# Kernel tuning notes

Hardware: AMD Instinct MI355X
Metric: run time of the kernel (lower is better)

The kernel has to match this reference:

```python
import jax, jax.numpy as jnp
import numpy as np

N = 10000      # nodes
E = 50000      # edges
NS = 48        # multiplicity of 0e (scalars)
NV = 10        # multiplicity of 1o (vectors)
NEF = 128      # n_edge_features
HID = 128      # hidden_features
W1N = NS * NS  # path 0e x 0e -> 0e
W2N = NS * NV  # path 0e x 1o -> 1o
W3N = NV * NV  # path 1o x 0e -> 1o
W4N = NV * NS  # path 1o x 1o -> 0e
WTOT = W1N + W2N + W3N + W4N  # tp.weight_numel = 3364
EPS = 1e-5
INV_SQRT3 = float(1.0 / np.sqrt(3.0))   # w3j(1,1,0) coefficient
NORM0 = float(1.0 / np.sqrt(NS + NV))   # path normalization into 0e output
NORM1 = float(1.0 / np.sqrt(NS + NV))   # path normalization into 1o output


def setup_inputs() -> dict:
    key = jax.random.key(0)
    ks = jax.random.split(key, 6)
    node_attr = jax.random.normal(ks[0], (N, NS + 3 * NV), jnp.float32)
    edge_index = jax.random.randint(ks[1], (2, E), 0, N, dtype=jnp.int32)
    edge_attr = jax.random.normal(ks[2], (E, NEF), jnp.float32)
    edge_sh = jax.random.normal(ks[3], (E, 4), jnp.float32)
    fc_w1 = jax.random.normal(ks[4], (NEF, HID), jnp.float32) / np.sqrt(NEF)
    fc_b1 = jnp.zeros((HID,), jnp.float32)
    fc_w2 = jax.random.normal(ks[5], (HID, WTOT), jnp.float32) / np.sqrt(HID)
    fc_b2 = jnp.zeros((WTOT,), jnp.float32)
    bn_weight = jnp.ones((NS + NV,), jnp.float32)  # affine scale per irrep
    bn_bias = jnp.zeros((NS,), jnp.float32)        # bias only for scalars
    return {"node_attr": node_attr, "edge_index": edge_index,
            "edge_attr": edge_attr, "edge_sh": edge_sh,
            "fc_w1": fc_w1, "fc_b1": fc_b1, "fc_w2": fc_w2, "fc_b2": fc_b2,
            "bn_weight": bn_weight, "bn_bias": bn_bias}


def reference(node_attr, edge_index, edge_attr, edge_sh,
              fc_w1, fc_b1, fc_w2, fc_b2, bn_weight, bn_bias):
    edge_src, edge_dst = edge_index[0], edge_index[1]

    # gather node features per edge
    x = node_attr[edge_dst]                       # [E, 78]
    s_in = x[:, :NS]                              # [E, NS] scalars (0e)
    v_in = x[:, NS:].reshape(E, NV, 3)            # [E, NV, 3] vectors (1o)
    sh0 = edge_sh[:, 0:1]                         # [E, 1]   sh 0e
    sh1 = edge_sh[:, 1:4]                         # [E, 3]   sh 1o

    # weight-generating MLP (per-edge tensor-product weights)
    h = jax.nn.relu(edge_attr @ fc_w1 + fc_b1)
    w = h @ fc_w2 + fc_b2                         # [E, 3364]
    w1 = w[:, :W1N].reshape(E, NS, NS)
    w2 = w[:, W1N:W1N + W2N].reshape(E, NS, NV)
    w3 = w[:, W1N + W2N:W1N + W2N + W3N].reshape(E, NV, NV)
    w4 = w[:, W1N + W2N + W3N:].reshape(E, NV, NS)

    # Clebsch-Gordan tensor product (4 paths)
    dot = jnp.einsum('evi,ei->ev', v_in, sh1) * INV_SQRT3      # 1o x 1o -> 0e
    out0 = (jnp.einsum('euv,eu->ev', w1, s_in) * sh0
            + jnp.einsum('euv,eu->ev', w4, dot)) * NORM0        # [E, NS]
    out1 = (jnp.einsum('euv,eu->ev', w2, s_in)[:, :, None] * sh1[:, None, :]
            + jnp.einsum('euv,eui->evi', w3, v_in) * sh0[:, :, None]) * NORM1  # [E, NV, 3]
    tp = jnp.concatenate([out0, out1.reshape(E, 3 * NV)], axis=-1)  # [E, 78]

    # scatter-mean to nodes
    summed = jax.ops.segment_sum(tp, edge_src, num_segments=N)
    cnt = jax.ops.segment_sum(jnp.ones((E,), tp.dtype), edge_src, num_segments=N)
    out = summed / jnp.maximum(cnt, 1.0)[:, None]

    # residual (in/out dims equal, so F.pad is a no-op)
    out = out + node_attr

    # e3nn-style equivariant BatchNorm (training mode, component normalization)
    s = out[:, :NS]
    v = out[:, NS:].reshape(N, NV, 3)
    s = s - s.mean(axis=0)
    s = s * jax.lax.rsqrt((s ** 2).mean(axis=0) + EPS) * bn_weight[:NS] + bn_bias
    vn = (v ** 2).mean(axis=-1).mean(axis=0)       # [NV] mean squared component
    v = v * (jax.lax.rsqrt(vn + EPS) * bn_weight[NS:])[None, :, None]
    return jnp.concatenate([s, v.reshape(N, 3 * NV)], axis=-1)
```

## Files before the change

kernel.cpp:

```cpp
#include <hip/hip_runtime.h>
#include <hip/hip_bf16.h>

#define NS 48
#define NV 10
#define NATT 78
#define HID 128
#define WTOT 3364
#define NEDGE 50000
#define NNODE 10000
#define EPAD 50048
#define EPSV 1e-5f
#define INV_SQRT3 0.57735026918962576f
#define NORM0 0.13130643285972254f
#define NORM1 0.13130643285972254f

#define FXS  2147483648.0f
#define FXSI (1.0 / 2147483648.0)
#define FXQ  268435456.0f
#define FXQI (1.0 / 268435456.0)

#define CPAD2 3744
#define NTILE 232
#define NGRP  78

#define NBLK_NODE 256

#define PREP_BLKS 1872
#define FC1_BLKS  782
#define ZERO_BYTES 6280000
#define ZERO_BLKS 1534

using half8 = __attribute__((ext_vector_type(8))) _Float16;
using f32x4 = __attribute__((ext_vector_type(4))) float;

__device__ __forceinline__ unsigned short f2h(float x) {
  union { _Float16 h; unsigned short u; } v;
  v.h = (_Float16)x;
  return v.u;
}

__device__ __forceinline__ void atomFx(unsigned long long* p, float x) {
  long long q = (long long)rintf(x * FXS);
  atomicAdd(p, (unsigned long long)q);
}

__device__ __forceinline__ int cp_to_src(int cp) {
  if (cp < 2304) return cp;
  if (cp < 2784) return 2884 + (cp - 2304);
  if (cp < 3552) { int t = cp - 2784; int u = t >> 4, v = t & 15;
                   return (v < 10) ? (2304 + u * 10 + v) : -1; }
  if (cp < 3712) { int t = cp - 3552; int u = t >> 4, v = t & 15;
                   return (v < 10) ? (2784 + u * 10 + v) : -1; }
  return -1;
}

__global__ __launch_bounds__(256) void k_front(const float* __restrict__ w2,
                                               unsigned short* __restrict__ Bt2,
                                               const float* __restrict__ ea,
                                               const float* __restrict__ w1,
                                               const float* __restrict__ b1,
                                               unsigned short* __restrict__ hbf,
                                               char* __restrict__ zbase) {
  __shared__ _Float16 w1T[128][136];
  const int bid = blockIdx.x;
  const int tid = threadIdx.x;

  if (bid < PREP_BLKS) {
    int idx = bid * 256 + tid;
    int cp = idx >> 7, k = idx & 127;
    int c_src = cp_to_src(cp);
    Bt2[idx] = (c_src >= 0) ? f2h(w2[(size_t)k * WTOT + c_src]) : (unsigned short)0;
    return;
  }
  if (bid >= PREP_BLKS + FC1_BLKS) {
    size_t off = ((size_t)(bid - PREP_BLKS - FC1_BLKS) * 256 + tid) * 16;
    if (off < ZERO_BYTES) *(uint4*)(zbase + off) = make_uint4(0, 0, 0, 0);
    return;
  }

  const int b  = bid - PREP_BLKS;
  const int e0 = b * 64;
  for (int i = tid; i < 128 * 128; i += 256) {
    int k = i >> 7, n = i & 127;
    w1T[n][k] = (_Float16)w1[i];
  }
  __syncthreads();

  const int lane = tid & 63, wid = tid >> 6;
  const int col = lane & 15, quad = lane >> 4;
  int e  = e0 + wid * 16 + col;
  int er = (e < NEDGE) ? e : 0;
  const float* ear = ea + (size_t)er * 128;
  half8 aF[4];
  #pragma unroll
  for (int ks = 0; ks < 4; ++ks) {
    float4 x0 = *(const float4*)&ear[ks * 32 + quad * 8];
    float4 x1 = *(const float4*)&ear[ks * 32 + quad * 8 + 4];
    half8 a;
    a[0] = (_Float16)x0.x; a[1] = (_Float16)x0.y; a[2] = (_Float16)x0.z; a[3] = (_Float16)x0.w;
    a[4] = (_Float16)x1.x; a[5] = (_Float16)x1.y; a[6] = (_Float16)x1.z; a[7] = (_Float16)x1.w;
    aF[ks] = a;
  }
  const int erow = e0 + wid * 16 + quad * 4;
  #pragma unroll
  for (int t = 0; t < 8; ++t) {
    float b1c = b1[t * 16 + col];
    f32x4 m = {0.f, 0.f, 0.f, 0.f};
    #pragma unroll
    for (int ks = 0; ks < 4; ++ks) {
      half8 bf = *(const half8*)&w1T[t * 16 + col][ks * 32 + quad * 8];
      m = __builtin_amdgcn_mfma_f32_16x16x32_f16(aF[ks], bf, m, 0, 0, 0);
    }
    #pragma unroll
    for (int r = 0; r < 4; ++r) {
      float h = fmaxf(m[r] + b1c, 0.f);
      hbf[(size_t)(erow + r) * 128 + t * 16 + col] = f2h(h);
    }
  }
}

__global__ __launch_bounds__(256, 3) void k_tp(const unsigned short* __restrict__ hbf,
                                               const unsigned short* __restrict__ Bt2,
                                               const float* __restrict__ fb2,
                                               const int* __restrict__ eidx,
                                               const float* __restrict__ node_attr,
                                               const float* __restrict__ esh,
                                               unsigned long long* __restrict__ summed,
                                               unsigned* __restrict__ cnt) {
  __shared__ half8    bufB[1536];
  __shared__ float    sFT[48][64];
  __shared__ float    vFL[64][30];
  __shared__ _Float16 b2pH[CPAD2];
  __shared__ float    p0FL[64], q0FL[64];
  __shared__ float    sh1nL[64][3];
  __shared__ int      srcL[64], dstL[64];

  const int tid  = threadIdx.x;
  const int wid  = tid >> 6;
  const int lane = tid & 63;
  const int col  = lane & 15;
  const int quad = lane >> 4;
  const int e0   = blockIdx.x * 64;
  const int elb  = wid * 16 + quad * 4;

  if (tid < 64) {
    int eg = e0 + tid;
    bool val = eg < NEDGE;
    srcL[tid] = val ? eidx[eg] : -1;
    dstL[tid] = val ? eidx[NEDGE + eg] : -1;
    float sh0 = 0.f, s1x = 0.f, s1y = 0.f, s1z = 0.f;
    if (val) {
      float4 s4 = *(const float4*)&esh[(size_t)eg * 4];
      sh0 = s4.x; s1x = s4.y; s1y = s4.z; s1z = s4.w;
    }
    p0FL[tid] = sh0 * NORM0;
    q0FL[tid] = sh0 * NORM1;
    sh1nL[tid][0] = s1x * NORM1; sh1nL[tid][1] = s1y * NORM1; sh1nL[tid][2] = s1z * NORM1;
  }
  for (int i = tid; i < CPAD2; i += 256) {
    int c_src = cp_to_src(i);
    b2pH[i] = (c_src >= 0) ? (_Float16)fb2[c_src] : (_Float16)0.f;
  }
  __syncthreads();
  for (int i = tid; i < 64 * NATT; i += 256) {
    int el = i / NATT, a = i % NATT;
    int dst = dstL[el];
    float x = (dst >= 0) ? node_attr[(size_t)dst * NATT + a] : 0.f;
    if (a < NS) sFT[a][el] = x; else vFL[el][a - NS] = x;
  }
  __syncthreads();

  half8 aF0, aF1, aF2, aF3;
  {
    const half8* hp = (const half8*)hbf;
    size_t arow = (size_t)(e0 + wid * 16 + col) * 16;
    aF0 = hp[arow + 0 * 4 + quad];
    aF1 = hp[arow + 1 * 4 + quad];
    aF2 = hp[arow + 2 * 4 + quad];
    aF3 = hp[arow + 3 * 4 + quad];
  }
  float p0v[4];
  #pragma unroll
  for (int r = 0; r < 4; ++r) p0v[r] = p0FL[elb + r];

  const char* bt2c = (const char*)Bt2;
  const int colS = tid >> 4, k8sS = tid & 15;
  const size_t gOff = (size_t)(colS * 16 + (k8sS ^ colS)) * 16;

  #define STAGE3(G) do {                                                           \
    int _t0 = (G) * 3;                                                             \
    char* _db = (char*)bufB + ((G) & 1) * 12288 + wid * 1024;                      \
    _Pragma("unroll")                                                              \
    for (int _t = 0; _t < 3; ++_t)                                                 \
      __builtin_amdgcn_global_load_lds(                                            \
        (const __attribute__((address_space(1))) void*)(bt2c + (size_t)(_t0 + _t) * 4096 + gOff), \
        (__attribute__((address_space(3))) void*)(_db + _t * 4096), 16, 0, 0);     \
  } while (0)

  STAGE3(0); STAGE3(1);

  float acc0[4][3] = {};
  float t1a[4] = {};
  float t3a[4][3] = {};

  const int k0 = (0 * 4 + quad) ^ col;
  const int k1 = (1 * 4 + quad) ^ col;
  const int k2 = (2 * 4 + quad) ^ col;
  const int k3 = (3 * 4 + quad) ^ col;
  const int cb = col * 16;

  #pragma unroll 1
  for (int p = 0; p < NGRP; ++p) {
    asm volatile("s_waitcnt vmcnt(0)\n\ts_barrier" ::: "memory");

    const int bb = ((p & 1) << 9) + ((p & 1) << 8) + cb;
    half8 b00 = bufB[bb +   0 + k0], b01 = bufB[bb +   0 + k1],
          b02 = bufB[bb +   0 + k2], b03 = bufB[bb +   0 + k3];
    half8 b10 = bufB[bb + 256 + k0], b11 = bufB[bb + 256 + k1],
          b12 = bufB[bb + 256 + k2], b13 = bufB[bb + 256 + k3];
    half8 b20 = bufB[bb + 512 + k0], b21 = bufB[bb + 512 + k1],
          b22 = bufB[bb + 512 + k2], b23 = bufB[bb + 512 + k3];

    __builtin_amdgcn_s_setprio(1);
    f32x4 m0 = {0.f, 0.f, 0.f, 0.f};
    f32x4 m1 = {0.f, 0.f, 0.f, 0.f};
    f32x4 m2 = {0.f, 0.f, 0.f, 0.f};
    m0 = __builtin_amdgcn_mfma_f32_16x16x32_f16(aF0, b00, m0, 0, 0, 0);
    m1 = __builtin_amdgcn_mfma_f32_16x16x32_f16(aF0, b10, m1, 0, 0, 0);
    m2 = __builtin_amdgcn_mfma_f32_16x16x32_f16(aF0, b20, m2, 0, 0, 0);
    m0 = __builtin_amdgcn_mfma_f32_16x16x32_f16(aF1, b01, m0, 0, 0, 0);
    m1 = __builtin_amdgcn_mfma_f32_16x16x32_f16(aF1, b11, m1, 0, 0, 0);
    m2 = __builtin_amdgcn_mfma_f32_16x16x32_f16(aF1, b21, m2, 0, 0, 0);
    m0 = __builtin_amdgcn_mfma_f32_16x16x32_f16(aF2, b02, m0, 0, 0, 0);
    m1 = __builtin_amdgcn_mfma_f32_16x16x32_f16(aF2, b12, m1, 0, 0, 0);
    m2 = __builtin_amdgcn_mfma_f32_16x16x32_f16(aF2, b22, m2, 0, 0, 0);
    m0 = __builtin_amdgcn_mfma_f32_16x16x32_f16(aF3, b03, m0, 0, 0, 0);
    m1 = __builtin_amdgcn_mfma_f32_16x16x32_f16(aF3, b13, m1, 0, 0, 0);
    m2 = __builtin_amdgcn_mfma_f32_16x16x32_f16(aF3, b23, m2, 0, 0, 0);
    __builtin_amdgcn_s_setprio(0);

    asm volatile("s_waitcnt lgkmcnt(0)\n\ts_barrier" ::: "memory");
    if (p < NGRP - 2) STAGE3(p + 2);

    float b2c0 = (float)b2pH[(p * 3 + 0) * 16 + col];
    float b2c1 = (float)b2pH[(p * 3 + 1) * 16 + col];
    float b2c2 = (float)b2pH[(p * 3 + 2) * 16 + col];
    if (p < 48) {
      #pragma unroll
      for (int r = 0; r < 4; ++r) {
        float sfac = sFT[p][elb + r] * p0v[r];
        acc0[r][0] += (m0[r] + b2c0) * sfac;
        acc0[r][1] += (m1[r] + b2c1) * sfac;
        acc0[r][2] += (m2[r] + b2c2) * sfac;
      }
    } else if (p < 58) {
      int u3 = (p - 48) * 3;
      #pragma unroll
      for (int r = 0; r < 4; ++r) {
        int el = elb + r;
        float dfac = (vFL[el][u3]     * sh1nL[el][0] +
                      vFL[el][u3 + 1] * sh1nL[el][1] +
                      vFL[el][u3 + 2] * sh1nL[el][2]) * INV_SQRT3;
        acc0[r][0] += (m0[r] + b2c0) * dfac;
        acc0[r][1] += (m1[r] + b2c1) * dfac;
        acc0[r][2] += (m2[r] + b2c2) * dfac;
      }
    } else if (p < 74) {
      int u0 = (p - 58) * 3;
      #pragma unroll
      for (int r = 0; r < 4; ++r) {
        int el = elb + r;
        t1a[r] += (m0[r] + b2c0) * sFT[u0][el]
                + (m1[r] + b2c1) * sFT[u0 + 1][el]
                + (m2[r] + b2c2) * sFT[u0 + 2][el];
      }
    } else {
      int ub = (p - 74) * 3;
      int T0 = p * 3;
      #pragma unroll
      for (int r = 0; r < 4; ++r) {
        int el = elb + r;
        {
          float w = m0[r] + b2c0;
          t3a[r][0] += w * vFL[el][(ub + 0) * 3 + 0];
          t3a[r][1] += w * vFL[el][(ub + 0) * 3 + 1];
          t3a[r][2] += w * vFL[el][(ub + 0) * 3 + 2];
        }
        if (T0 + 1 < NTILE) {
          float w = m1[r] + b2c1;
          t3a[r][0] += w * vFL[el][(ub + 1) * 3 + 0];
          t3a[r][1] += w * vFL[el][(ub + 1) * 3 + 1];
          t3a[r][2] += w * vFL[el][(ub + 1) * 3 + 2];
        }
        if (T0 + 2 < NTILE) {
          float w = m2[r] + b2c2;
          t3a[r][0] += w * vFL[el][(ub + 2) * 3 + 0];
          t3a[r][1] += w * vFL[el][(ub + 2) * 3 + 1];
          t3a[r][2] += w * vFL[el][(ub + 2) * 3 + 2];
        }
      }
    }
  }
  #undef STAGE3

  #pragma unroll
  for (int r = 0; r < 4; ++r) {
    int el = elb + r;
    int src = srcL[el];
    if (src < 0) continue;
    unsigned long long* dp = &summed[(size_t)src * NATT];
    #pragma unroll
    for (int j = 0; j < 3; ++j)
      atomFx(dp + j * 16 + col, acc0[r][j]);
    if (col < 10) {
      float q0 = q0FL[el];
      #pragma unroll
      for (int i = 0; i < 3; ++i)
        atomFx(dp + NS + col * 3 + i,
               t1a[r] * sh1nL[el][i] + t3a[r][i] * q0);
    }
  }
  if (tid < 64 && srcL[tid] >= 0) atomicAdd(&cnt[srcL[tid]], 1u);
}

__global__ __launch_bounds__(256) void k_node(const unsigned long long* __restrict__ summed,
                                              const unsigned* __restrict__ cnt,
                                              const float* __restrict__ node_attr,
                                              float* __restrict__ outp,
                                              unsigned long long* __restrict__ partials) {
  __shared__ unsigned long long ls[NS], lq[NS], lv[NV];
  int tid = threadIdx.x;
  if (tid < NS) { ls[tid] = 0ull; lq[tid] = 0ull; }
  if (tid < NV) lv[tid] = 0ull;
  __syncthreads();
  for (int i = blockIdx.x * 256 + tid; i < NNODE * NATT; i += NBLK_NODE * 256) {
    int row = i / NATT, colc = i % NATT;
    long long sv = (long long)summed[i];
    float sum = (float)((double)sv * FXSI);
    float x = sum / fmaxf((float)cnt[row], 1.f) + node_attr[i];
    outp[i] = x;
    if (colc < NS) {
      atomicAdd(&ls[colc], (unsigned long long)(long long)rintf(x * FXS));
      atomicAdd(&lq[colc], (unsigned long long)(long long)rintf(x * x * FXQ));
    } else {
      atomicAdd(&lv[(colc - NS) / 3], (unsigned long long)(long long)rintf(x * x * FXQ));
    }
  }
  __syncthreads();
  if (tid < 128) {
    unsigned long long v = 0ull;
    if (tid < NS)            v = ls[tid];
    else if (tid < 2 * NS)   v = lq[tid - NS];
    else if (tid < 96 + NV)  v = lv[tid - 96];
    partials[(size_t)blockIdx.x * 128 + tid] = v;
  }
}

__global__ __launch_bounds__(128) void k_stats(const unsigned long long* __restrict__ partials,
                                               unsigned long long* __restrict__ stats) {
  int c = threadIdx.x;
  unsigned long long s = 0ull;
  for (int b = 0; b < NBLK_NODE; ++b) s += partials[(size_t)b * 128 + c];
  stats[c] = s;
}

__global__ __launch_bounds__(256) void k_bn(const float* __restrict__ outp,
                                            const unsigned long long* __restrict__ stats,
                                            const float* __restrict__ bnw,
                                            const float* __restrict__ bnb,
                                            float* __restrict__ out) {
  int i = blockIdx.x * 256 + threadIdx.x;
  if (i >= NNODE * NATT) return;
  int colc = i % NATT;
  float x = outp[i];
  float r;
  if (colc < NS) {
    float mean = (float)((double)(long long)stats[colc] * (FXSI / NNODE));
    float ex2  = (float)((double)(long long)stats[NS + colc] * (FXQI / NNODE));
    float var  = ex2 - mean * mean;
    r = (x - mean) * rsqrtf(var + EPSV) * bnw[colc] + bnb[colc];
  } else {
    int u = (colc - NS) / 3;
    float vn = (float)((double)(long long)stats[96 + u] * (FXQI / (3.0 * NNODE)));
    r = x * rsqrtf(vn + EPSV) * bnw[NS + u];
  }
  out[i] = r;
}

extern "C" void kernel_launch(void* const* d_in, const int* in_sizes, int n_in,
                              void* d_out, int out_size, void* d_ws, size_t ws_size,
                              hipStream_t stream) {
  const float* node_attr = (const float*)d_in[0];
  const int*   eidx      = (const int*)d_in[1];
  const float* edge_attr = (const float*)d_in[2];
  const float* esh       = (const float*)d_in[3];
  const float* fw1       = (const float*)d_in[4];
  const float* fb1       = (const float*)d_in[5];
  const float* fw2       = (const float*)d_in[6];
  const float* fb2       = (const float*)d_in[7];
  const float* bnw       = (const float*)d_in[8];
  const float* bnb       = (const float*)d_in[9];
  float* out = (float*)d_out;

  char* ws = (char*)d_ws;
  unsigned short*     Bt2      = (unsigned short*)(ws + 0);
  unsigned short*     hbf      = (unsigned short*)(ws + 958464);
  unsigned long long* summed   = (unsigned long long*)(ws + 13770752);
  unsigned*           cnt      = (unsigned*)(ws + 20010752);
  float*              outp     = (float*)(ws + 0);
  unsigned long long* partials = (unsigned long long*)(ws + 3120000);
  unsigned long long* stats    = (unsigned long long*)(ws + 3382144);

  k_front<<<PREP_BLKS + FC1_BLKS + ZERO_BLKS, 256, 0, stream>>>(
      fw2, Bt2, edge_attr, fw1, fb1, hbf, ws + 13770752);
  k_tp<<<EPAD / 64, 256, 0, stream>>>(hbf, Bt2, fb2, eidx, node_attr, esh, summed, cnt);
  k_node<<<NBLK_NODE, 256, 0, stream>>>(summed, cnt, node_attr, outp, partials);
  k_stats<<<1, 128, 0, stream>>>(partials, stats);
  int nelem_blocks = (NNODE * NATT + 255) / 256;
  k_bn<<<nelem_blocks, 256, 0, stream>>>(outp, stats, bnw, bnb, out);
}
```

Baseline: 293.8 us.

## Double edges per tensor-product block so eight waves share staged weight tiles

```diff
diff --git a/kernel.cpp b/kernel.cpp
--- a/kernel.cpp
+++ b/kernel.cpp
@@ -29,6 +29,8 @@
 #define FC1_BLKS  782
 #define ZERO_BYTES 6280000
 #define ZERO_BLKS 1534
+
+#define TP_BLKS 391
 
 using half8 = __attribute__((ext_vector_type(8))) _Float16;
 using f32x4 = __attribute__((ext_vector_type(4))) float;
@@ -119,7 +121,7 @@
   }
 }
 
-__global__ __launch_bounds__(256, 3) void k_tp(const unsigned short* __restrict__ hbf,
+__global__ __launch_bounds__(512, 4) void k_tp(const unsigned short* __restrict__ hbf,
                                                const unsigned short* __restrict__ Bt2,
                                                const float* __restrict__ fb2,
                                                const int* __restrict__ eidx,
@@ -128,45 +130,44 @@
                                                unsigned long long* __restrict__ summed,
                                                unsigned* __restrict__ cnt) {
   __shared__ half8    bufB[1536];
-  __shared__ float    sFT[48][64];
-  __shared__ float    vFL[64][30];
+  __shared__ _Float16 sFT[48][128];
+  __shared__ _Float16 vFL[128][30];
   __shared__ _Float16 b2pH[CPAD2];
-  __shared__ float    p0FL[64], q0FL[64];
-  __shared__ float    sh1nL[64][3];
-  __shared__ int      srcL[64], dstL[64];
 
   const int tid  = threadIdx.x;
   const int wid  = tid >> 6;
   const int lane = tid & 63;
   const int col  = lane & 15;
   const int quad = lane >> 4;
-  const int e0   = blockIdx.x * 64;
+  const int e0   = blockIdx.x * 128;
   const int elb  = wid * 16 + quad * 4;
 
-  if (tid < 64) {
-    int eg = e0 + tid;
+  float p0v[4];
+  float sh1n[4][3];
+  int   srcR[4];
+  #pragma unroll
+  for (int r = 0; r < 4; ++r) {
+    int eg = e0 + elb + r;
     bool val = eg < NEDGE;
-    srcL[tid] = val ? eidx[eg] : -1;
-    dstL[tid] = val ? eidx[NEDGE + eg] : -1;
-    float sh0 = 0.f, s1x = 0.f, s1y = 0.f, s1z = 0.f;
+    srcR[r] = val ? eidx[eg] : -1;
+    float sh0 = 0.f, x = 0.f, y = 0.f, z = 0.f;
     if (val) {
       float4 s4 = *(const float4*)&esh[(size_t)eg * 4];
-      sh0 = s4.x; s1x = s4.y; s1y = s4.z; s1z = s4.w;
-    }
-    p0FL[tid] = sh0 * NORM0;
-    q0FL[tid] = sh0 * NORM1;
-    sh1nL[tid][0] = s1x * NORM1; sh1nL[tid][1] = s1y * NORM1; sh1nL[tid][2] = s1z * NORM1;
-  }
-  for (int i = tid; i < CPAD2; i += 256) {
+      sh0 = s4.x; x = s4.y; y = s4.z; z = s4.w;
+    }
+    p0v[r] = sh0 * NORM0;
+    sh1n[r][0] = x * NORM1; sh1n[r][1] = y * NORM1; sh1n[r][2] = z * NORM1;
+  }
+  for (int i = tid; i < CPAD2; i += 512) {
     int c_src = cp_to_src(i);
     b2pH[i] = (c_src >= 0) ? (_Float16)fb2[c_src] : (_Float16)0.f;
   }
-  __syncthreads();
-  for (int i = tid; i < 64 * NATT; i += 256) {
+  for (int i = tid; i < 128 * NATT; i += 512) {
     int el = i / NATT, a = i % NATT;
-    int dst = dstL[el];
+    int eg = e0 + el;
+    int dst = (eg < NEDGE) ? eidx[NEDGE + eg] : -1;
     float x = (dst >= 0) ? node_attr[(size_t)dst * NATT + a] : 0.f;
-    if (a < NS) sFT[a][el] = x; else vFL[el][a - NS] = x;
+    if (a < NS) sFT[a][el] = (_Float16)x; else vFL[el][a - NS] = (_Float16)x;
   }
   __syncthreads();
 
@@ -179,22 +180,21 @@
     aF2 = hp[arow + 2 * 4 + quad];
     aF3 = hp[arow + 3 * 4 + quad];
   }
-  float p0v[4];
-  #pragma unroll
-  for (int r = 0; r < 4; ++r) p0v[r] = p0FL[elb + r];
 
   const char* bt2c = (const char*)Bt2;
-  const int colS = tid >> 4, k8sS = tid & 15;
+  const int colS = (tid >> 4) & 15, k8sS = tid & 15;
   const size_t gOff = (size_t)(colS * 16 + (k8sS ^ colS)) * 16;
 
   #define STAGE3(G) do {                                                           \
-    int _t0 = (G) * 3;                                                             \
-    char* _db = (char*)bufB + ((G) & 1) * 12288 + wid * 1024;                      \
-    _Pragma("unroll")                                                              \
-    for (int _t = 0; _t < 3; ++_t)                                                 \
-      __builtin_amdgcn_global_load_lds(                                            \
-        (const __attribute__((address_space(1))) void*)(bt2c + (size_t)(_t0 + _t) * 4096 + gOff), \
-        (__attribute__((address_space(3))) void*)(_db + _t * 4096), 16, 0, 0);     \
+    if (wid < 4) {                                                                 \
+      int _t0 = (G) * 3;                                                           \
+      char* _db = (char*)bufB + ((G) & 1) * 12288 + wid * 1024;                    \
+      _Pragma("unroll")                                                            \
+      for (int _t = 0; _t < 3; ++_t)                                               \
+        __builtin_amdgcn_global_load_lds(                                          \
+          (const __attribute__((address_space(1))) void*)(bt2c + (size_t)(_t0 + _t) * 4096 + gOff), \
+          (__attribute__((address_space(3))) void*)(_db + _t * 4096), 16, 0, 0);   \
+    }                                                                              \
   } while (0)
 
   STAGE3(0); STAGE3(1);
@@ -248,7 +248,7 @@
     if (p < 48) {
       #pragma unroll
       for (int r = 0; r < 4; ++r) {
-        float sfac = sFT[p][elb + r] * p0v[r];
+        float sfac = (float)sFT[p][elb + r] * p0v[r];
         acc0[r][0] += (m0[r] + b2c0) * sfac;
         acc0[r][1] += (m1[r] + b2c1) * sfac;
         acc0[r][2] += (m2[r] + b2c2) * sfac;
@@ -258,9 +258,9 @@
       #pragma unroll
       for (int r = 0; r < 4; ++r) {
         int el = elb + r;
-        float dfac = (vFL[el][u3]     * sh1nL[el][0] +
-                      vFL[el][u3 + 1] * sh1nL[el][1] +
-                      vFL[el][u3 + 2] * sh1nL[el][2]) * INV_SQRT3;
+        float dfac = ((float)vFL[el][u3]     * sh1n[r][0] +
+                      (float)vFL[el][u3 + 1] * sh1n[r][1] +
+                      (float)vFL[el][u3 + 2] * sh1n[r][2]) * INV_SQRT3;
         acc0[r][0] += (m0[r] + b2c0) * dfac;
         acc0[r][1] += (m1[r] + b2c1) * dfac;
         acc0[r][2] += (m2[r] + b2c2) * dfac;
@@ -270,9 +270,9 @@
       #pragma unroll
       for (int r = 0; r < 4; ++r) {
         int el = elb + r;
-        t1a[r] += (m0[r] + b2c0) * sFT[u0][el]
-                + (m1[r] + b2c1) * sFT[u0 + 1][el]
-                + (m2[r] + b2c2) * sFT[u0 + 2][el];
+        t1a[r] += (m0[r] + b2c0) * (float)sFT[u0][el]
+                + (m1[r] + b2c1) * (float)sFT[u0 + 1][el]
+                + (m2[r] + b2c2) * (float)sFT[u0 + 2][el];
       }
     } else {
       int ub = (p - 74) * 3;
@@ -282,21 +282,21 @@
         int el = elb + r;
         {
           float w = m0[r] + b2c0;
-          t3a[r][0] += w * vFL[el][(ub + 0) * 3 + 0];
-          t3a[r][1] += w * vFL[el][(ub + 0) * 3 + 1];
-          t3a[r][2] += w * vFL[el][(ub + 0) * 3 + 2];
+          t3a[r][0] += w * (float)vFL[el][(ub + 0) * 3 + 0];
+          t3a[r][1] += w * (float)vFL[el][(ub + 0) * 3 + 1];
+          t3a[r][2] += w * (float)vFL[el][(ub + 0) * 3 + 2];
         }
         if (T0 + 1 < NTILE) {
           float w = m1[r] + b2c1;
-          t3a[r][0] += w * vFL[el][(ub + 1) * 3 + 0];
-          t3a[r][1] += w * vFL[el][(ub + 1) * 3 + 1];
-          t3a[r][2] += w * vFL[el][(ub + 1) * 3 + 2];
+          t3a[r][0] += w * (float)vFL[el][(ub + 1) * 3 + 0];
+          t3a[r][1] += w * (float)vFL[el][(ub + 1) * 3 + 1];
+          t3a[r][2] += w * (float)vFL[el][(ub + 1) * 3 + 2];
         }
         if (T0 + 2 < NTILE) {
           float w = m2[r] + b2c2;
-          t3a[r][0] += w * vFL[el][(ub + 2) * 3 + 0];
-          t3a[r][1] += w * vFL[el][(ub + 2) * 3 + 1];
-          t3a[r][2] += w * vFL[el][(ub + 2) * 3 + 2];
+          t3a[r][0] += w * (float)vFL[el][(ub + 2) * 3 + 0];
+          t3a[r][1] += w * (float)vFL[el][(ub + 2) * 3 + 1];
+          t3a[r][2] += w * (float)vFL[el][(ub + 2) * 3 + 2];
         }
       }
     }
@@ -305,22 +305,24 @@
 
   #pragma unroll
   for (int r = 0; r < 4; ++r) {
-    int el = elb + r;
-    int src = srcL[el];
+    int src = srcR[r];
     if (src < 0) continue;
     unsigned long long* dp = &summed[(size_t)src * NATT];
     #pragma unroll
     for (int j = 0; j < 3; ++j)
       atomFx(dp + j * 16 + col, acc0[r][j]);
     if (col < 10) {
-      float q0 = q0FL[el];
+      float q0 = p0v[r];
       #pragma unroll
       for (int i = 0; i < 3; ++i)
         atomFx(dp + NS + col * 3 + i,
-               t1a[r] * sh1nL[el][i] + t3a[r][i] * q0);
-    }
-  }
-  if (tid < 64 && srcL[tid] >= 0) atomicAdd(&cnt[srcL[tid]], 1u);
+               t1a[r] * sh1n[r][i] + t3a[r][i] * q0);
+    }
+  }
+  if (tid < 128) {
+    int eg = e0 + tid;
+    if (eg < NEDGE) atomicAdd(&cnt[eidx[eg]], 1u);
+  }
 }
 
 __global__ __launch_bounds__(256) void k_node(const unsigned long long* __restrict__ summed,
@@ -413,7 +415,7 @@
 
   k_front<<<PREP_BLKS + FC1_BLKS + ZERO_BLKS, 256, 0, stream>>>(
       fw2, Bt2, edge_attr, fw1, fb1, hbf, ws + 13770752);
-  k_tp<<<EPAD / 64, 256, 0, stream>>>(hbf, Bt2, fb2, eidx, node_attr, esh, summed, cnt);
+  k_tp<<<TP_BLKS, 512, 0, stream>>>(hbf, Bt2, fb2, eidx, node_attr, esh, summed, cnt);
   k_node<<<NBLK_NODE, 256, 0, stream>>>(summed, cnt, node_attr, outp, partials);
   k_stats<<<1, 128, 0, stream>>>(partials, stats);
   int nelem_blocks = (NNODE * NATT + 255) / 256;
```

Measured after the change: 270.5 us. 7.9% less time.
